# Kernel tuning notes

Hardware: AMD Instinct MI355X
Metric: run time of the kernel (lower is better)

The kernel has to match this reference:

```python
import jax, jax.numpy as jnp
import numpy as np

CH = 512


def _maxpool2(t):
    # 2x2 max pool, stride 2, NCHW
    B, C, H, W = t.shape
    return t.reshape(B, C, H // 2, 2, W // 2, 2).max(axis=(3, 5))


def setup_inputs() -> dict:
    key = jax.random.key(0)
    ks = jax.random.split(key, 6)
    B, C, H, W = 8, CH, 64, 64
    x = jax.random.normal(ks[0], (B, C, H, W), dtype=jnp.float32)
    # 1x1 conv weights stored as [out_ch, in_ch]
    w_theta = jax.random.normal(ks[1], (C // 8, C), dtype=jnp.float32) * (1.0 / np.sqrt(C))
    w_phi = jax.random.normal(ks[2], (C // 8, C), dtype=jnp.float32) * (1.0 / np.sqrt(C))
    w_g = jax.random.normal(ks[3], (C // 2, C), dtype=jnp.float32) * (1.0 / np.sqrt(C))
    w_o = jax.random.normal(ks[4], (C, C // 2), dtype=jnp.float32) * (1.0 / np.sqrt(C // 2))
    # gamma is a learned scalar (init 0.0 in the original); use 0.5 so the
    # attention branch contributes to the output for testing purposes.
    gamma = jnp.float32(0.5)
    return {"x": x, "w_theta": w_theta, "w_phi": w_phi, "w_g": w_g, "w_o": w_o, "gamma": gamma}


def reference(x, w_theta, w_phi, w_g, w_o, gamma):
    B, C, H, W = x.shape
    c8, c2 = C // 8, C // 2
    # 1x1 conv projections
    theta = jnp.einsum('bchw,oc->bohw', x, w_theta)           # [B, C/8, H, W]
    phi = _maxpool2(jnp.einsum('bchw,oc->bohw', x, w_phi))    # [B, C/8, H/2, W/2]
    g = _maxpool2(jnp.einsum('bchw,oc->bohw', x, w_g))        # [B, C/2, H/2, W/2]
    n, m = H * W, (H * W) // 4
    theta = theta.reshape(B, c8, n)
    phi = phi.reshape(B, c8, m)
    g = g.reshape(B, c2, m)
    # unscaled attention scores: [B, n, m]
    beta = jax.nn.softmax(jnp.einsum('bcn,bcm->bnm', theta, phi), axis=-1)
    # attend: g @ beta^T -> [B, C/2, n]
    att = jnp.einsum('bcm,bnm->bcn', g, beta).reshape(B, c2, H, W)
    o = jnp.einsum('bchw,oc->bohw', att, w_o)                 # [B, C, H, W]
    return gamma * o + x
```

## Files before the change

kernel.cpp:

```cpp
#include <hip/hip_runtime.h>
#include <math.h>

constexpr int CB = 8;
constexpr int CC = 512;
constexpr int CN = 4096;
constexpr int CM = 1024;
constexpr int C8 = 64;
constexpr int C2 = 256;

typedef __attribute__((ext_vector_type(8))) short short8;
typedef __attribute__((ext_vector_type(8))) _Float16 half8;
typedef __attribute__((ext_vector_type(4))) float f32x4;

__device__ inline unsigned short f2bf(float f) {
  unsigned int u = __float_as_uint(f);
  return (unsigned short)((u + 0x7FFFu + ((u >> 16) & 1u)) >> 16);
}
__device__ inline unsigned short f16bits(float f) {
  union { _Float16 h; unsigned short u; } c;
  c.h = (_Float16)f;
  return c.u;
}

__global__ __launch_bounds__(256)
void conv_w(const float* __restrict__ wt, const float* __restrict__ wp,
            const float* __restrict__ wg, const float* __restrict__ wo,
            _Float16* __restrict__ wth, _Float16* __restrict__ wtl,
            _Float16* __restrict__ wph, _Float16* __restrict__ wpl,
            _Float16* __restrict__ wgf, unsigned short* __restrict__ woh) {
  const int i = blockIdx.x * 256 + threadIdx.x;
  if (i < 32768) {
    float a = wt[i];
    _Float16 h = (_Float16)a;
    wth[i] = h; wtl[i] = (_Float16)(a - (float)h);
    a = wp[i];
    h = (_Float16)a;
    wph[i] = h; wpl[i] = (_Float16)(a - (float)h);
  }
  wgf[i] = (_Float16)wg[i];
  woh[i] = f2bf(wo[i]);
}

__global__ __launch_bounds__(256)
void xpose(const float* __restrict__ X, _Float16* __restrict__ xT) {
  __shared__ __align__(16) float raw[64][68];
  const int b = blockIdx.z, c0 = blockIdx.y * 64, n0 = blockIdx.x * 64;
  const float* Xb = X + ((size_t)b * CC + c0) * CN + n0;
  const int tid = threadIdx.x;
#pragma unroll
  for (int it = 0; it < 4; ++it) {
    const int idx = it * 256 + tid;
    const int row = idx >> 4, col4 = (idx & 15) * 4;
    *(float4*)&raw[row][col4] = *(const float4*)&Xb[(size_t)row * CN + col4];
  }
  __syncthreads();
  unsigned short* Yb = (unsigned short*)(xT + ((size_t)b * CN + n0) * CC + c0);
#pragma unroll
  for (int it = 0; it < 4; ++it) {
    const int idx = it * 256 + tid;
    const int n = idx >> 4, c4 = (idx & 15) * 4;
    ushort4 o;
    o.x = f16bits(raw[c4 + 0][n]);
    o.y = f16bits(raw[c4 + 1][n]);
    o.z = f16bits(raw[c4 + 2][n]);
    o.w = f16bits(raw[c4 + 3][n]);
    *(ushort4*)&Yb[(size_t)n * CC + c4] = o;
  }
}

__global__ __launch_bounds__(256)
void proj_th(const _Float16* __restrict__ Wh, const _Float16* __restrict__ Wl,
             const _Float16* __restrict__ xT, _Float16* __restrict__ thT) {
  __shared__ __align__(16) unsigned short LT[64][68];
  const int b = blockIdx.y, n0 = blockIdx.x * 64;
  const int tid = threadIdx.x;
  const int w = tid >> 6, l = tid & 63;
  const int l15 = l & 15, quad = l >> 4;
  f32x4 acc[4] = {};
  const _Float16* Brow = xT + (size_t)(b * CN + n0 + w * 16 + l15) * CC;
  for (int k0 = 0; k0 < CC; k0 += 32) {
    const half8 bfr = *(const half8*)&Brow[k0 + quad * 8];
#pragma unroll
    for (int i = 0; i < 4; ++i) {
      const half8 ah = *(const half8*)&Wh[(size_t)(i * 16 + l15) * CC + k0 + quad * 8];
      const half8 al = *(const half8*)&Wl[(size_t)(i * 16 + l15) * CC + k0 + quad * 8];
      acc[i] = __builtin_amdgcn_mfma_f32_16x16x32_f16(ah, bfr, acc[i], 0, 0, 0);
      acc[i] = __builtin_amdgcn_mfma_f32_16x16x32_f16(al, bfr, acc[i], 0, 0, 0);
    }
  }
#pragma unroll
  for (int i = 0; i < 4; ++i)
#pragma unroll
    for (int r = 0; r < 4; ++r)
      LT[w * 16 + l15][i * 16 + quad * 4 + r] = f16bits(acc[i][r]);
  __syncthreads();
  unsigned short* Yb = (unsigned short*)(thT + (size_t)(b * CN + n0) * C8);
#pragma unroll
  for (int it = 0; it < 4; ++it) {
    const int idx = it * 256 + tid;
    const int pos = idx >> 4, c4 = (idx & 15) * 4;
    ushort4 v = *(const ushort4*)&LT[pos][c4];
    *(ushort4*)&Yb[(size_t)pos * C8 + c4] = v;
  }
}

__global__ __launch_bounds__(256)
void proj_pg(const _Float16* __restrict__ Wph, const _Float16* __restrict__ Wpl,
             const _Float16* __restrict__ Wg, const _Float16* __restrict__ xT,
             _Float16* __restrict__ phT, unsigned short* __restrict__ gbf) {
  __shared__ float Pbuf[2][64][33];
  const int b = blockIdx.z, mt = blockIdx.y, tile = blockIdx.x;
  const int n0 = tile * 256;
  const int tid = threadIdx.x;
  const int w = tid >> 6, l = tid & 63;
  const int l15 = l & 15, quad = l >> 4;
  const bool isphi = (mt == 0);
  const _Float16* Ah = isphi ? Wph : (Wg + (size_t)(mt - 1) * 64 * CC);
  f32x4 acc[4][4] = {};
  const _Float16* Bbase = xT + (size_t)(b * CN + n0 + w * 64) * CC;
  for (int k0 = 0; k0 < CC; k0 += 32) {
    half8 bf[4], ah[4];
#pragma unroll
    for (int j = 0; j < 4; ++j)
      bf[j] = *(const half8*)&Bbase[(size_t)(j * 16 + l15) * CC + k0 + quad * 8];
#pragma unroll
    for (int i = 0; i < 4; ++i)
      ah[i] = *(const half8*)&Ah[(size_t)(i * 16 + l15) * CC + k0 + quad * 8];
#pragma unroll
    for (int i = 0; i < 4; ++i)
#pragma unroll
      for (int j = 0; j < 4; ++j)
        acc[i][j] = __builtin_amdgcn_mfma_f32_16x16x32_f16(ah[i], bf[j], acc[i][j], 0, 0, 0);
    if (isphi) {
      half8 al[4];
#pragma unroll
      for (int i = 0; i < 4; ++i)
        al[i] = *(const half8*)&Wpl[(size_t)(i * 16 + l15) * CC + k0 + quad * 8];
#pragma unroll
      for (int i = 0; i < 4; ++i)
#pragma unroll
        for (int j = 0; j < 4; ++j)
          acc[i][j] = __builtin_amdgcn_mfma_f32_16x16x32_f16(al[i], bf[j], acc[i][j], 0, 0, 0);
    }
  }
  const bool owner = ((l15 & 1) == 0);
  const int colh = l15 >> 1;
  if (w & 1) {
#pragma unroll
    for (int i = 0; i < 4; ++i)
#pragma unroll
      for (int j = 0; j < 4; ++j)
#pragma unroll
        for (int r = 0; r < 4; ++r) {
          float v = acc[i][j][r];
          float o = __shfl_xor(v, 1);
          v = fmaxf(v, o);
          if (owner) Pbuf[w >> 1][i * 16 + quad * 4 + r][j * 8 + colh] = v;
        }
  }
  __syncthreads();
  if (!(w & 1)) {
    const int pr = tile * 2 + (w >> 1);
    unsigned short* phB = (unsigned short*)(phT + ((size_t)b * CM + pr * 32) * C8);
#pragma unroll
    for (int i = 0; i < 4; ++i)
#pragma unroll
      for (int j = 0; j < 4; ++j)
#pragma unroll
        for (int r = 0; r < 4; ++r) {
          float v = acc[i][j][r];
          float o = __shfl_xor(v, 1);
          v = fmaxf(v, o);
          if (owner) {
            const int oc = i * 16 + quad * 4 + r;
            const int col = j * 8 + colh;
            v = fmaxf(v, Pbuf[w >> 1][oc][col]);
            if (isphi)
              phB[(size_t)col * C8 + oc] = f16bits(v);
            else
              gbf[((size_t)b * C2 + (mt - 1) * 64 + oc) * CM + pr * 32 + col] = f2bf(v);
          }
        }
  }
}

__global__ __launch_bounds__(256)
void attn_v4(const _Float16* __restrict__ thT, const _Float16* __restrict__ phT,
             const unsigned short* __restrict__ gbf,
             unsigned short* __restrict__ attbf) {
  __shared__ __align__(16) unsigned short Pl[2][4][16][40];
  __shared__ float Dinv[64];
  const int b = blockIdx.y;
  const int q0 = blockIdx.x * 64;
  const int tid = threadIdx.x;
  const int w = tid >> 6, l = tid & 63;
  const int l15 = l & 15, quad = l >> 4;
  half8 tb[2];
#pragma unroll
  for (int kc = 0; kc < 2; ++kc)
    tb[kc] = *(const half8*)&thT[(size_t)(b * CN + q0 + w * 16 + l15) * C8 +
                                 kc * 32 + quad * 8];
  f32x4 acc[4][4] = {};
  float dnp = 0.f;
  const _Float16* phB = phT + (size_t)b * CM * C8;
  const unsigned short* gB = gbf + (size_t)b * C2 * CM;

  for (int j0 = 0; j0 < CM; j0 += 32) {
    const int buf = (j0 >> 5) & 1;
    short8 gf[4];
#pragma unroll
    for (int ct = 0; ct < 4; ++ct)
      gf[ct] = *(const short8*)&gB[(size_t)(w * 64 + ct * 16 + l15) * CM +
                                   j0 + quad * 8];
    half8 pa[2][2];
#pragma unroll
    for (int jt = 0; jt < 2; ++jt)
#pragma unroll
      for (int kc = 0; kc < 2; ++kc)
        pa[jt][kc] = *(const half8*)&phB[(size_t)(j0 + jt * 16 + l15) * C8 +
                                         kc * 32 + quad * 8];
    f32x4 S0 = {0.f, 0.f, 0.f, 0.f}, S1 = {0.f, 0.f, 0.f, 0.f};
    S0 = __builtin_amdgcn_mfma_f32_16x16x32_f16(pa[0][0], tb[0], S0, 0, 0, 0);
    S0 = __builtin_amdgcn_mfma_f32_16x16x32_f16(pa[0][1], tb[1], S0, 0, 0, 0);
    S1 = __builtin_amdgcn_mfma_f32_16x16x32_f16(pa[1][0], tb[0], S1, 0, 0, 0);
    S1 = __builtin_amdgcn_mfma_f32_16x16x32_f16(pa[1][1], tb[1], S1, 0, 0, 0);
    float e0[4], e1[4];
#pragma unroll
    for (int r = 0; r < 4; ++r) { e0[r] = __expf(S0[r]); e1[r] = __expf(S1[r]); }
    dnp += (e0[0] + e0[1]) + (e0[2] + e0[3]) +
           (e1[0] + e1[1]) + (e1[2] + e1[3]);
    ushort4 w0, w1;
    w0.x = f2bf(e0[0]); w0.y = f2bf(e0[1]); w0.z = f2bf(e0[2]); w0.w = f2bf(e0[3]);
    w1.x = f2bf(e1[0]); w1.y = f2bf(e1[1]); w1.z = f2bf(e1[2]); w1.w = f2bf(e1[3]);
    *(ushort4*)&Pl[buf][w][l15][quad * 4] = w0;
    *(ushort4*)&Pl[buf][w][l15][16 + quad * 4] = w1;
    __syncthreads();
    short8 pfrag[4];
#pragma unroll
    for (int qs = 0; qs < 4; ++qs)
      pfrag[qs] = *(const short8*)&Pl[buf][qs][l15][quad * 8];
#pragma unroll
    for (int ct = 0; ct < 4; ++ct)
#pragma unroll
      for (int qs = 0; qs < 4; ++qs)
        acc[qs][ct] = __builtin_amdgcn_mfma_f32_16x16x32_bf16(pfrag[qs], gf[ct],
                                                              acc[qs][ct], 0, 0, 0);
  }
  float d = dnp;
  d += __shfl_xor(d, 16);
  d += __shfl_xor(d, 32);
  if (quad == 0) Dinv[w * 16 + l15] = 1.0f / d;
  __syncthreads();
  unsigned short* attB = attbf + (size_t)(b * CN + q0) * C2;
#pragma unroll
  for (int qs = 0; qs < 4; ++qs) {
#pragma unroll
    for (int r = 0; r < 4; ++r) {
      const int row = qs * 16 + quad * 4 + r;
      const float iv = Dinv[row];
#pragma unroll
      for (int ct = 0; ct < 4; ++ct)
        attB[(size_t)row * C2 + w * 64 + ct * 16 + l15] =
            f2bf(acc[qs][ct][r] * iv);
    }
  }
}

__global__ __launch_bounds__(256, 8)
void oproj_v2(const unsigned short* __restrict__ woh,
              const unsigned short* __restrict__ attbf,
              const float* __restrict__ X, const float* __restrict__ gamma,
              float* __restrict__ out) {
  __shared__ __align__(16) float Tw[4][16][34];
  const int b = blockIdx.z;
  const int mt = blockIdx.y;
  const int n0 = blockIdx.x * 64;
  const int tid = threadIdx.x;
  const int w = tid >> 6, l = tid & 63;
  const int l15 = l & 15, quad = l >> 4;
  const int wc = w >> 1, wn = w & 1;
  const int cbase = mt * 64 + wc * 32;
  const int nbase = n0 + wn * 32;
  const unsigned short* Bb = attbf + (size_t)b * CN * C2;
  f32x4 acc[2][2] = {};
  for (int k0 = 0; k0 < C2; k0 += 32) {
    short8 a[2], bb[2];
#pragma unroll
    for (int i = 0; i < 2; ++i)
      a[i] = *(const short8*)&woh[(size_t)(cbase + i * 16 + l15) * C2 + k0 + quad * 8];
#pragma unroll
    for (int j = 0; j < 2; ++j)
      bb[j] = *(const short8*)&Bb[(size_t)(nbase + j * 16 + l15) * C2 + k0 + quad * 8];
#pragma unroll
    for (int i = 0; i < 2; ++i)
#pragma unroll
      for (int j = 0; j < 2; ++j)
        acc[i][j] = __builtin_amdgcn_mfma_f32_16x16x32_bf16(a[i], bb[j], acc[i][j], 0, 0, 0);
  }
  const float gm = gamma[0];
  const int cp = l >> 2;
  const int nq = (l & 3) * 8;
#pragma unroll
  for (int i = 0; i < 2; ++i) {
#pragma unroll
    for (int j = 0; j < 2; ++j)
#pragma unroll
      for (int r = 0; r < 4; ++r)
        Tw[w][quad * 4 + r][j * 16 + l15] = acc[i][j][r];
    const float4 v0 = *(const float4*)&Tw[w][cp][nq];
    const float4 v1 = *(const float4*)&Tw[w][cp][nq + 4];
    const int c = cbase + i * 16 + cp;
    const size_t idx = ((size_t)b * CC + c) * CN + nbase + nq;
    const float4 x0 = *(const float4*)&X[idx];
    const float4 x1 = *(const float4*)&X[idx + 4];
    float4 o0, o1;
    o0.x = x0.x + gm * v0.x; o0.y = x0.y + gm * v0.y;
    o0.z = x0.z + gm * v0.z; o0.w = x0.w + gm * v0.w;
    o1.x = x1.x + gm * v1.x; o1.y = x1.y + gm * v1.y;
    o1.z = x1.z + gm * v1.z; o1.w = x1.w + gm * v1.w;
    *(float4*)&out[idx] = o0;
    *(float4*)&out[idx + 4] = o1;
    __syncthreads();
  }
}

extern "C" void kernel_launch(void* const* d_in, const int* in_sizes, int n_in,
                              void* d_out, int out_size, void* d_ws, size_t ws_size,
                              hipStream_t stream) {
  const float* x       = (const float*)d_in[0];
  const float* w_theta = (const float*)d_in[1];
  const float* w_phi   = (const float*)d_in[2];
  const float* w_g     = (const float*)d_in[3];
  const float* w_o     = (const float*)d_in[4];
  const float* gamma   = (const float*)d_in[5];
  float* out = (float*)d_out;
  char* wsb = (char*)d_ws;

  _Float16*       xT    = (_Float16*)(wsb + 0);
  _Float16*       thT   = (_Float16*)(wsb + 33554432);
  _Float16*       phT   = (_Float16*)(wsb + 37748736);
  unsigned short* gbf   = (unsigned short*)(wsb + 38797312);
  _Float16*       wth   = (_Float16*)(wsb + 42991616);
  _Float16*       wtl   = (_Float16*)(wsb + 43057152);
  _Float16*       wph   = (_Float16*)(wsb + 43122688);
  _Float16*       wpl   = (_Float16*)(wsb + 43188224);
  _Float16*       wgf   = (_Float16*)(wsb + 43253760);
  unsigned short* woh   = (unsigned short*)(wsb + 43515904);
  unsigned short* attbf = (unsigned short*)(wsb + 0);

  dim3 blk(256);
  conv_w<<<512, blk, 0, stream>>>(w_theta, w_phi, w_g, w_o,
                                  wth, wtl, wph, wpl, wgf, woh);
  xpose<<<dim3(64, 8, CB), blk, 0, stream>>>(x, xT);
  proj_th<<<dim3(64, CB), blk, 0, stream>>>(wth, wtl, xT, thT);
  proj_pg<<<dim3(16, 5, CB), blk, 0, stream>>>(wph, wpl, wgf, xT, phT, gbf);
  attn_v4<<<dim3(64, CB), blk, 0, stream>>>(thT, phT, gbf, attbf);
  oproj_v2<<<dim3(64, 8, CB), blk, 0, stream>>>(woh, attbf, x, gamma, out);
}
```

Measured before the change: 338.5 us.

## Double-buffer loads in projection and attention kernels, retile theta projection

The theta projection gets smaller tiles (32 positions per block, twice the blocks) and preloads all of its K-fragments of x into registers. The phi/g projection and attention loops are double-buffered, so the next chunk's global loads are issued before the current chunk's MFMAs. The output projection preloads every A/B fragment up front, writes both halves into a doubled LDS buffer, and drops a per-iteration barrier. Together these aim to hide global-load latency and add parallelism, at the cost of higher register pressure that may lower occupancy.

```diff
diff --git a/kernel.cpp b/kernel.cpp
--- a/kernel.cpp
+++ b/kernel.cpp
@@ -68,35 +68,43 @@
   }
 }
 
-__global__ __launch_bounds__(256)
-void proj_th(const _Float16* __restrict__ Wh, const _Float16* __restrict__ Wl,
-             const _Float16* __restrict__ xT, _Float16* __restrict__ thT) {
-  __shared__ __align__(16) unsigned short LT[64][68];
-  const int b = blockIdx.y, n0 = blockIdx.x * 64;
+__global__ __launch_bounds__(256, 2)
+void proj_th2(const _Float16* __restrict__ Wh, const _Float16* __restrict__ Wl,
+              const _Float16* __restrict__ xT, _Float16* __restrict__ thT) {
+  __shared__ __align__(16) unsigned short LT[32][68];
+  const int b = blockIdx.y, n0 = blockIdx.x * 32;
   const int tid = threadIdx.x;
   const int w = tid >> 6, l = tid & 63;
   const int l15 = l & 15, quad = l >> 4;
-  f32x4 acc[4] = {};
-  const _Float16* Brow = xT + (size_t)(b * CN + n0 + w * 16 + l15) * CC;
-  for (int k0 = 0; k0 < CC; k0 += 32) {
-    const half8 bfr = *(const half8*)&Brow[k0 + quad * 8];
-#pragma unroll
-    for (int i = 0; i < 4; ++i) {
-      const half8 ah = *(const half8*)&Wh[(size_t)(i * 16 + l15) * CC + k0 + quad * 8];
-      const half8 al = *(const half8*)&Wl[(size_t)(i * 16 + l15) * CC + k0 + quad * 8];
-      acc[i] = __builtin_amdgcn_mfma_f32_16x16x32_f16(ah, bfr, acc[i], 0, 0, 0);
-      acc[i] = __builtin_amdgcn_mfma_f32_16x16x32_f16(al, bfr, acc[i], 0, 0, 0);
+  const int wn = w & 1, wo = w >> 1;
+  const _Float16* Brow = xT + (size_t)(b * CN + n0 + wn * 16 + l15) * CC;
+  half8 bfr[16];
+#pragma unroll
+  for (int kk = 0; kk < 16; ++kk)
+    bfr[kk] = *(const half8*)&Brow[kk * 32 + quad * 8];
+  f32x4 acc[2] = {};
+#pragma unroll
+  for (int kk = 0; kk < 16; ++kk) {
+    const int k0 = kk * 32;
+#pragma unroll
+    for (int i = 0; i < 2; ++i) {
+      const half8 ah = *(const half8*)&Wh[(size_t)(wo * 32 + i * 16 + l15) * CC +
+                                          k0 + quad * 8];
+      const half8 al = *(const half8*)&Wl[(size_t)(wo * 32 + i * 16 + l15) * CC +
+                                          k0 + quad * 8];
+      acc[i] = __builtin_amdgcn_mfma_f32_16x16x32_f16(ah, bfr[kk], acc[i], 0, 0, 0);
+      acc[i] = __builtin_amdgcn_mfma_f32_16x16x32_f16(al, bfr[kk], acc[i], 0, 0, 0);
     }
   }
 #pragma unroll
-  for (int i = 0; i < 4; ++i)
+  for (int i = 0; i < 2; ++i)
 #pragma unroll
     for (int r = 0; r < 4; ++r)
-      LT[w * 16 + l15][i * 16 + quad * 4 + r] = f16bits(acc[i][r]);
+      LT[wn * 16 + l15][wo * 32 + i * 16 + quad * 4 + r] = f16bits(acc[i][r]);
   __syncthreads();
   unsigned short* Yb = (unsigned short*)(thT + (size_t)(b * CN + n0) * C8);
 #pragma unroll
-  for (int it = 0; it < 4; ++it) {
+  for (int it = 0; it < 2; ++it) {
     const int idx = it * 256 + tid;
     const int pos = idx >> 4, c4 = (idx & 15) * 4;
     ushort4 v = *(const ushort4*)&LT[pos][c4];
@@ -118,11 +126,14 @@
   const _Float16* Ah = isphi ? Wph : (Wg + (size_t)(mt - 1) * 64 * CC);
   f32x4 acc[4][4] = {};
   const _Float16* Bbase = xT + (size_t)(b * CN + n0 + w * 64) * CC;
-  for (int k0 = 0; k0 < CC; k0 += 32) {
-    half8 bf[4], ah[4];
+
+  auto loadB = [&](half8 (&bf)[4], int k0) {
 #pragma unroll
     for (int j = 0; j < 4; ++j)
       bf[j] = *(const half8*)&Bbase[(size_t)(j * 16 + l15) * CC + k0 + quad * 8];
+  };
+  auto doK = [&](half8 (&bf)[4], int k0) {
+    half8 ah[4];
 #pragma unroll
     for (int i = 0; i < 4; ++i)
       ah[i] = *(const half8*)&Ah[(size_t)(i * 16 + l15) * CC + k0 + quad * 8];
@@ -142,6 +153,15 @@
         for (int j = 0; j < 4; ++j)
           acc[i][j] = __builtin_amdgcn_mfma_f32_16x16x32_f16(al[i], bf[j], acc[i][j], 0, 0, 0);
     }
+  };
+
+  half8 bfA[4], bfB[4];
+  loadB(bfA, 0);
+  for (int k0 = 0; k0 < CC; k0 += 64) {
+    loadB(bfB, k0 + 32);
+    doK(bfA, k0);
+    if (k0 + 64 < CC) loadB(bfA, k0 + 64);
+    doK(bfB, k0 + 32);
   }
   const bool owner = ((l15 & 1) == 0);
   const int colh = l15 >> 1;
@@ -184,8 +204,8 @@
   }
 }
 
-__global__ __launch_bounds__(256)
-void attn_v4(const _Float16* __restrict__ thT, const _Float16* __restrict__ phT,
+__global__ __launch_bounds__(256, 2)
+void attn_v6(const _Float16* __restrict__ thT, const _Float16* __restrict__ phT,
              const unsigned short* __restrict__ gbf,
              unsigned short* __restrict__ attbf) {
   __shared__ __align__(16) unsigned short Pl[2][4][16][40];
@@ -205,20 +225,19 @@
   const _Float16* phB = phT + (size_t)b * CM * C8;
   const unsigned short* gB = gbf + (size_t)b * C2 * CM;
 
-  for (int j0 = 0; j0 < CM; j0 += 32) {
-    const int buf = (j0 >> 5) & 1;
-    short8 gf[4];
+  auto loadc = [&](half8 (&pa)[2][2], short8 (&gf)[4], int j0) {
 #pragma unroll
     for (int ct = 0; ct < 4; ++ct)
       gf[ct] = *(const short8*)&gB[(size_t)(w * 64 + ct * 16 + l15) * CM +
                                    j0 + quad * 8];
-    half8 pa[2][2];
 #pragma unroll
     for (int jt = 0; jt < 2; ++jt)
 #pragma unroll
       for (int kc = 0; kc < 2; ++kc)
         pa[jt][kc] = *(const half8*)&phB[(size_t)(j0 + jt * 16 + l15) * C8 +
                                          kc * 32 + quad * 8];
+  };
+  auto step = [&](half8 (&pa)[2][2], short8 (&gf)[4], int buf) {
     f32x4 S0 = {0.f, 0.f, 0.f, 0.f}, S1 = {0.f, 0.f, 0.f, 0.f};
     S0 = __builtin_amdgcn_mfma_f32_16x16x32_f16(pa[0][0], tb[0], S0, 0, 0, 0);
     S0 = __builtin_amdgcn_mfma_f32_16x16x32_f16(pa[0][1], tb[1], S0, 0, 0, 0);
@@ -245,6 +264,16 @@
       for (int qs = 0; qs < 4; ++qs)
         acc[qs][ct] = __builtin_amdgcn_mfma_f32_16x16x32_bf16(pfrag[qs], gf[ct],
                                                               acc[qs][ct], 0, 0, 0);
+  };
+
+  half8 paA[2][2], paB[2][2];
+  short8 gfA[4], gfB[4];
+  loadc(paA, gfA, 0);
+  for (int j0 = 0; j0 < CM; j0 += 64) {
+    loadc(paB, gfB, j0 + 32);
+    step(paA, gfA, 0);
+    if (j0 + 64 < CM) loadc(paA, gfA, j0 + 64);
+    step(paB, gfB, 1);
   }
   float d = dnp;
   d += __shfl_xor(d, 16);
@@ -266,12 +295,12 @@
   }
 }
 
-__global__ __launch_bounds__(256, 8)
-void oproj_v2(const unsigned short* __restrict__ woh,
+__global__ __launch_bounds__(256, 3)
+void oproj_v3(const unsigned short* __restrict__ woh,
               const unsigned short* __restrict__ attbf,
               const float* __restrict__ X, const float* __restrict__ gamma,
               float* __restrict__ out) {
-  __shared__ __align__(16) float Tw[4][16][34];
+  __shared__ __align__(16) float Tw[2][4][16][34];
   const int b = blockIdx.z;
   const int mt = blockIdx.y;
   const int n0 = blockIdx.x * 64;
@@ -282,33 +311,41 @@
   const int cbase = mt * 64 + wc * 32;
   const int nbase = n0 + wn * 32;
   const unsigned short* Bb = attbf + (size_t)b * CN * C2;
+  short8 a[8][2], bb[8][2];
+#pragma unroll
+  for (int ks = 0; ks < 8; ++ks) {
+#pragma unroll
+    for (int i = 0; i < 2; ++i)
+      a[ks][i] = *(const short8*)&woh[(size_t)(cbase + i * 16 + l15) * C2 +
+                                      ks * 32 + quad * 8];
+#pragma unroll
+    for (int j = 0; j < 2; ++j)
+      bb[ks][j] = *(const short8*)&Bb[(size_t)(nbase + j * 16 + l15) * C2 +
+                                      ks * 32 + quad * 8];
+  }
   f32x4 acc[2][2] = {};
-  for (int k0 = 0; k0 < C2; k0 += 32) {
-    short8 a[2], bb[2];
+#pragma unroll
+  for (int ks = 0; ks < 8; ++ks)
 #pragma unroll
     for (int i = 0; i < 2; ++i)
-      a[i] = *(const short8*)&woh[(size_t)(cbase + i * 16 + l15) * C2 + k0 + quad * 8];
-#pragma unroll
-    for (int j = 0; j < 2; ++j)
-      bb[j] = *(const short8*)&Bb[(size_t)(nbase + j * 16 + l15) * C2 + k0 + quad * 8];
-#pragma unroll
-    for (int i = 0; i < 2; ++i)
 #pragma unroll
       for (int j = 0; j < 2; ++j)
-        acc[i][j] = __builtin_amdgcn_mfma_f32_16x16x32_bf16(a[i], bb[j], acc[i][j], 0, 0, 0);
-  }
+        acc[i][j] = __builtin_amdgcn_mfma_f32_16x16x32_bf16(a[ks][i], bb[ks][j],
+                                                            acc[i][j], 0, 0, 0);
   const float gm = gamma[0];
   const int cp = l >> 2;
   const int nq = (l & 3) * 8;
 #pragma unroll
+  for (int i = 0; i < 2; ++i)
+#pragma unroll
+    for (int j = 0; j < 2; ++j)
+#pragma unroll
+      for (int r = 0; r < 4; ++r)
+        Tw[i][w][quad * 4 + r][j * 16 + l15] = acc[i][j][r];
+#pragma unroll
   for (int i = 0; i < 2; ++i) {
-#pragma unroll
-    for (int j = 0; j < 2; ++j)
-#pragma unroll
-      for (int r = 0; r < 4; ++r)
-        Tw[w][quad * 4 + r][j * 16 + l15] = acc[i][j][r];
-    const float4 v0 = *(const float4*)&Tw[w][cp][nq];
-    const float4 v1 = *(const float4*)&Tw[w][cp][nq + 4];
+    const float4 v0 = *(const float4*)&Tw[i][w][cp][nq];
+    const float4 v1 = *(const float4*)&Tw[i][w][cp][nq + 4];
     const int c = cbase + i * 16 + cp;
     const size_t idx = ((size_t)b * CC + c) * CN + nbase + nq;
     const float4 x0 = *(const float4*)&X[idx];
@@ -320,7 +357,6 @@
     o1.z = x1.z + gm * v1.z; o1.w = x1.w + gm * v1.w;
     *(float4*)&out[idx] = o0;
     *(float4*)&out[idx + 4] = o1;
-    __syncthreads();
   }
 }
 
@@ -352,8 +388,8 @@
   conv_w<<<512, blk, 0, stream>>>(w_theta, w_phi, w_g, w_o,
                                   wth, wtl, wph, wpl, wgf, woh);
   xpose<<<dim3(64, 8, CB), blk, 0, stream>>>(x, xT);
-  proj_th<<<dim3(64, CB), blk, 0, stream>>>(wth, wtl, xT, thT);
+  proj_th2<<<dim3(128, CB), blk, 0, stream>>>(wth, wtl, xT, thT);
   proj_pg<<<dim3(16, 5, CB), blk, 0, stream>>>(wph, wpl, wgf, xT, phT, gbf);
-  attn_v4<<<dim3(64, CB), blk, 0, stream>>>(thT, phT, gbf, attbf);
-  oproj_v2<<<dim3(64, 8, CB), blk, 0, stream>>>(woh, attbf, x, gamma, out);
-}
+  attn_v6<<<dim3(64, CB), blk, 0, stream>>>(thT, phT, gbf, attbf);
+  oproj_v3<<<dim3(64, 8, CB), blk, 0, stream>>>(woh, attbf, x, gamma, out);
+}
```

New measurement: 345.3 us. +2.0%, slower.
